# Kernel tuning notes

Measured on AMD Instinct MI355X. Metric: run time of the kernel, lower is better.

The kernel has to match this reference:

```python
import jax, jax.numpy as jnp
import numpy as np

EPS_BN = 1e-5
SLOPE = 0.2
K_SCALES = (5, 20, 30)
K_BRANCH = 20


def _pairwise(x):
    # x: [B, C, N] -> negative squared distances [B, N, N]
    inner = -2.0 * jnp.einsum('bcn,bcm->bnm', x, x)
    xx = jnp.sum(x * x, axis=1)  # [B, N]
    return -xx[:, :, None] - inner - xx[:, None, :]


def _gather(xt, idx):
    # xt: [B, N, C], idx: [B, N, k] -> [B, N, k, C]
    B = xt.shape[0]
    return xt[jnp.arange(B)[:, None, None], idx]


def _bn(x, g, b):
    # eval-mode BN: running_mean=0, running_var=1
    sh = (1, -1) + (1,) * (x.ndim - 2)
    return x * (g / jnp.sqrt(1.0 + EPS_BN)).reshape(sh) + b.reshape(sh)


def _conv(x, w, g, b):
    # 1x1 conv (no bias) + BN + LeakyReLU; x: [B, Cin, ...], w: [Cout, Cin]
    y = jnp.einsum('oc,bc...->bo...', w, x)
    return jax.nn.leaky_relu(_bn(y, g, b), SLOPE)


def _edge_feature(x, k):
    # DGCNN edge feature: cat(neighbor - center, center) -> [B, 2C, N, k]
    idx = jax.lax.top_k(_pairwise(x), k)[1]
    xt = jnp.transpose(x, (0, 2, 1))  # [B, N, C]
    nb = _gather(xt, idx)             # [B, N, k, C]
    ctr = jnp.broadcast_to(xt[:, :, None, :], nb.shape)
    return jnp.transpose(jnp.concatenate([nb - ctr, ctr], axis=-1), (0, 3, 1, 2))


def _hierarchical_features(x):
    pd = _pairwise(x)
    xt = jnp.transpose(x, (0, 2, 1))  # [B, N, 3]
    feats = []
    for scale, k in enumerate(K_SCALES):
        idx = jax.lax.top_k(pd, k)[1]
        nb = _gather(xt, idx)
        ctr = jnp.broadcast_to(xt[:, :, None, :], nb.shape)
        rel = nb - ctr
        if scale == 0:
            f = jnp.concatenate([rel, ctr], axis=-1)                         # 6 ch
        elif scale == 1:
            n = jnp.linalg.norm(rel, axis=-1, keepdims=True) + 1e-8
            f = jnp.concatenate([rel, rel / n, ctr], axis=-1)                # 9 ch
        else:
            d = jnp.linalg.norm(rel, axis=-1, keepdims=True)
            f = jnp.concatenate([rel, ctr, d], axis=-1)                      # 7 ch
        feats.append(jnp.transpose(f, (0, 3, 1, 2)))  # [B, C, N, k]
    return feats


def _forward(x, w1l, g1l, b1l, w1b, g1b, b1b, w1c, g1c, b1c,
             wf, gf, bf, w2, g2, b2, w3, g3, b3, w4, g4, b4,
             w5, g5, b5, wl1, g6, b6, wl2, bl2, g7, b7, wl3, bl3):
    fL, fB, fC = _hierarchical_features(x)
    xl = jnp.max(_conv(fL, w1l, g1l, b1l), axis=-1)   # [B, 64, N]
    xb = jnp.max(_conv(fB, w1b, g1b, b1b), axis=-1)
    xc = jnp.max(_conv(fC, w1c, g1c, b1c), axis=-1)
    xm = jnp.concatenate([xl, xb, xc], axis=1)        # [B, 192, N]
    x1 = _conv(xm, wf, gf, bf)                        # [B, 64, N]
    e = _edge_feature(x1, K_BRANCH)
    x2 = jnp.max(_conv(e, w2, g2, b2), axis=-1)       # [B, 64, N]
    e = _edge_feature(x2, K_BRANCH)
    x3 = jnp.max(_conv(e, w3, g3, b3), axis=-1)       # [B, 128, N]
    e = _edge_feature(x3, K_BRANCH)
    x4 = jnp.max(_conv(e, w4, g4, b4), axis=-1)       # [B, 256, N]
    xcat = jnp.concatenate([x1, x2, x3, x4], axis=1)  # [B, 512, N]
    x5 = _conv(xcat, w5, g5, b5)                      # [B, emb, N]
    h = jnp.concatenate([jnp.max(x5, axis=-1), jnp.mean(x5, axis=-1)], axis=1)  # [B, 2*emb]
    h = jax.nn.leaky_relu(_bn(h @ wl1.T, g6, b6), SLOPE)          # [B, 512]
    h = jax.nn.leaky_relu(_bn(h @ wl2.T + bl2, g7, b7), SLOPE)    # [B, 256]
    return h @ wl3.T + bl3                                        # [B, 7]


def setup_inputs() -> dict:
    key = jax.random.key(0)
    ks = jax.random.split(key, 64)
    it = iter(range(64))
    def W(shape):
        return 0.05 * jax.random.normal(ks[next(it)], shape, jnp.float32)
    def G(n):
        return 1.0 + 0.1 * jax.random.normal(ks[next(it)], (n,), jnp.float32)
    def Bt(n):
        return 0.1 * jax.random.normal(ks[next(it)], (n,), jnp.float32)
    emb = 1024
    inp = {
        'x': jax.random.normal(ks[next(it)], (16, 3, 2048), jnp.float32),
        'w1l': W((64, 6)),  'g1l': G(64),  'b1l': Bt(64),
        'w1b': W((64, 9)),  'g1b': G(64),  'b1b': Bt(64),
        'w1c': W((64, 7)),  'g1c': G(64),  'b1c': Bt(64),
        'wf': W((64, 192)), 'gf': G(64),   'bf': Bt(64),
        'w2': W((64, 128)), 'g2': G(64),   'b2': Bt(64),
        'w3': W((128, 128)),'g3': G(128),  'b3': Bt(128),
        'w4': W((256, 256)),'g4': G(256),  'b4': Bt(256),
        'w5': W((emb, 512)),'g5': G(emb),  'b5': Bt(emb),
        'wl1': W((512, 2 * emb)), 'g6': G(512), 'b6': Bt(512),
        'wl2': W((256, 512)), 'bl2': Bt(256), 'g7': G(256), 'b7': Bt(256),
        'wl3': W((7, 256)), 'bl3': Bt(7),
    }
    return inp


def reference(x, w1l, g1l, b1l, w1b, g1b, b1b, w1c, g1c, b1c,
              wf, gf, bf, w2, g2, b2, w3, g3, b3, w4, g4, b4,
              w5, g5, b5, wl1, g6, b6, wl2, bl2, g7, b7, wl3, bl3):
    return _forward(x, w1l, g1l, b1l, w1b, g1b, b1b, w1c, g1c, b1c,
                    wf, gf, bf, w2, g2, b2, w3, g3, b3, w4, g4, b4,
                    w5, g5, b5, wl1, g6, b6, wl2, bl2, g7, b7, wl3, bl3)
```

## Files before the change

kernel.cpp:

```cpp
#include <hip/hip_runtime.h>
#include <math.h>

#define BB 16
#define NN 2048
#define BN (BB * NN)
#define XS 512

typedef unsigned short u16;
typedef __attribute__((ext_vector_type(8))) short short8;
typedef __attribute__((ext_vector_type(4))) float f32x4;

__device__ __forceinline__ float leaky(float z) { return z > 0.f ? z : 0.2f * z; }
__device__ __forceinline__ float bnscale(float g) { return g / sqrtf(1.f + 1e-5f); }

template<int K>
__device__ __forceinline__ void wave_topk(float lv[32], int lane, int* out) {
    unsigned pop = 0u;
    float v1 = -INFINITY, v2 = -INFINITY, v3 = -INFINITY;
    int m1 = 0, m2 = 0, m3 = 0;
    #pragma unroll
    for (int m = 0; m < 32; ++m) {
        float v = lv[m];
        bool c1 = v > v1, c2 = v > v2, c3 = v > v3;
        v3 = c2 ? v2 : (c3 ? v : v3);
        m3 = c2 ? m2 : (c3 ? m : m3);
        v2 = c1 ? v1 : (c2 ? v : v2);
        m2 = c1 ? m1 : (c2 ? m : m2);
        v1 = c1 ? v : v1;
        m1 = c1 ? m : m1;
    }
    int nvalid = 3;
    #pragma unroll 1
    for (int k = 0; k < K; k += 2) {
        float a1 = v1, a2 = v2;
        int   g1 = m1 * 64 + lane, g2 = m2 * 64 + lane;
        #pragma unroll
        for (int off = 1; off < 64; off <<= 1) {
            float b1 = __shfl_xor(a1, off), b2 = __shfl_xor(a2, off);
            int   h1 = __shfl_xor(g1, off), h2 = __shfl_xor(g2, off);
            bool aw = (a1 > b1) || (a1 == b1 && g1 < h1);
            float w1  = aw ? a1 : b1;  int wi1 = aw ? g1 : h1;
            float lo  = aw ? b1 : a1;  int loi = aw ? h1 : g1;
            float ws  = aw ? a2 : b2;  int wsi = aw ? g2 : h2;
            bool sw = (lo > ws) || (lo == ws && loi < wsi);
            a1 = w1; g1 = wi1;
            a2 = sw ? lo : ws; g2 = sw ? loi : wsi;
        }
        if (lane == 0) {
            out[k] = g1;
            if (k + 1 < K) out[k + 1] = g2;
        }
        if (k + 2 >= K) break;
        const int myg1 = m1 * 64 + lane, myg2 = m2 * 64 + lane;
        const bool p1 = (myg1 == g1) || (myg1 == g2);
        const bool p2 = (myg2 == g1) || (myg2 == g2);
        if (p1) pop |= 1u << m1;
        if (p2) pop |= 1u << m2;
        const int np = (int)p1 + (int)p2;
        if (np == 2) {
            v1 = v3; m1 = m3;
        } else if (p1) {
            v1 = v2; m1 = m2; v2 = v3; m2 = m3;
        } else if (p2) {
            v2 = v3; m2 = m3;
        }
        nvalid -= np;
        if (nvalid < 2) {
            v1 = -INFINITY; v2 = -INFINITY; v3 = -INFINITY;
            m1 = 0; m2 = 0; m3 = 0;
            #pragma unroll
            for (int m = 0; m < 32; ++m) {
                float v = ((pop >> m) & 1u) ? -INFINITY : lv[m];
                bool c1 = v > v1, c2 = v > v2, c3 = v > v3;
                v3 = c2 ? v2 : (c3 ? v : v3);
                m3 = c2 ? m2 : (c3 ? m : m3);
                v2 = c1 ? v1 : (c2 ? v : v2);
                m2 = c1 ? m1 : (c2 ? m : m2);
                v1 = c1 ? v : v1;
                m1 = c1 ? m : m1;
            }
            nvalid = 3;
        }
    }
}

__global__ __launch_bounds__(256) void topk_xyz(const float* __restrict__ x,
                                                int* __restrict__ idx30) {
    const int tile = blockIdx.x;
    const int b = tile >> 9;
    const int i0 = (tile & 511) * 4;
    __shared__ float dist[4][NN];
    const float* xb = x + (size_t)b * 3 * NN;
    float xi[4][3], ni[4];
    #pragma unroll
    for (int t = 0; t < 4; ++t) {
        xi[t][0] = xb[i0 + t];
        xi[t][1] = xb[NN + i0 + t];
        xi[t][2] = xb[2 * NN + i0 + t];
        ni[t] = xi[t][0] * xi[t][0] + xi[t][1] * xi[t][1] + xi[t][2] * xi[t][2];
    }
    for (int j = threadIdx.x; j < NN; j += 256) {
        float a0 = xb[j], a1 = xb[NN + j], a2 = xb[2 * NN + j];
        float nj = a0 * a0 + a1 * a1 + a2 * a2;
        #pragma unroll
        for (int t = 0; t < 4; ++t) {
            float dot = xi[t][0] * a0 + xi[t][1] * a1 + xi[t][2] * a2;
            dist[t][j] = 2.f * dot - ni[t] - nj;
        }
    }
    __syncthreads();
    const int w = threadIdx.x >> 6;
    const int lane = threadIdx.x & 63;
    float lv[32];
    #pragma unroll
    for (int m = 0; m < 32; ++m) lv[m] = dist[w][m * 64 + lane];
    wave_topk<30>(lv, lane, idx30 + ((size_t)b * NN + i0 + w) * 30);
}

__global__ __launch_bounds__(64) void hier_conv(
        const float* __restrict__ x, const int* __restrict__ idx30,
        const float* __restrict__ w1l, const float* __restrict__ g1l, const float* __restrict__ b1l,
        const float* __restrict__ w1b, const float* __restrict__ g1b, const float* __restrict__ b1b,
        const float* __restrict__ w1c, const float* __restrict__ g1c, const float* __restrict__ b1c,
        const float* __restrict__ wf,  const float* __restrict__ gf,  const float* __restrict__ bf_,
        float* __restrict__ x1out) {
    const int bi = blockIdx.x;
    const int b = bi >> 11;
    const int i = bi & (NN - 1);
    const int o = threadIdx.x;
    __shared__ float xm[192];
    __shared__ float xjs[30][3];
    const float* xb = x + (size_t)b * 3 * NN;
    float xi0 = xb[i], xi1 = xb[NN + i], xi2 = xb[2 * NN + i];
    if (o < 30) {
        int j = idx30[(size_t)bi * 30 + o];
        xjs[o][0] = xb[j]; xjs[o][1] = xb[NN + j]; xjs[o][2] = xb[2 * NN + j];
    }
    float wl[6], wb[9], wc[7];
    #pragma unroll
    for (int c = 0; c < 6; ++c) wl[c] = w1l[o * 6 + c];
    #pragma unroll
    for (int c = 0; c < 9; ++c) wb[c] = w1b[o * 9 + c];
    #pragma unroll
    for (int c = 0; c < 7; ++c) wc[c] = w1c[o * 7 + c];
    float sl = bnscale(g1l[o]), bl = b1l[o];
    float sb = bnscale(g1b[o]), bbv = b1b[o];
    float sc = bnscale(g1c[o]), bc = b1c[o];
    __syncthreads();
    float aL = -INFINITY, aB = -INFINITY, aC = -INFINITY;
    for (int k = 0; k < 30; ++k) {
        float r0 = xjs[k][0] - xi0, r1 = xjs[k][1] - xi1, r2 = xjs[k][2] - xi2;
        float ss = r0 * r0 + r1 * r1 + r2 * r2;
        if (k < 5) {
            float y = wl[0]*r0 + wl[1]*r1 + wl[2]*r2 + wl[3]*xi0 + wl[4]*xi1 + wl[5]*xi2;
            aL = fmaxf(aL, leaky(y * sl + bl));
        }
        if (k < 20) {
            float nrm = sqrtf(ss) + 1e-8f;
            float y = wb[0]*r0 + wb[1]*r1 + wb[2]*r2
                    + wb[3]*(r0/nrm) + wb[4]*(r1/nrm) + wb[5]*(r2/nrm)
                    + wb[6]*xi0 + wb[7]*xi1 + wb[8]*xi2;
            aB = fmaxf(aB, leaky(y * sb + bbv));
        }
        {
            float d = sqrtf(ss);
            float y = wc[0]*r0 + wc[1]*r1 + wc[2]*r2 + wc[3]*xi0 + wc[4]*xi1 + wc[5]*xi2 + wc[6]*d;
            aC = fmaxf(aC, leaky(y * sc + bc));
        }
    }
    xm[o] = aL; xm[64 + o] = aB; xm[128 + o] = aC;
    __syncthreads();
    const float* wr = wf + (size_t)o * 192;
    float y = 0.f;
    #pragma unroll 8
    for (int c = 0; c < 192; c += 4) {
        float4 wv = *(const float4*)(wr + c);
        float4 xv = *(const float4*)(&xm[c]);
        y += wv.x * xv.x + wv.y * xv.y + wv.z * xv.z + wv.w * xv.w;
    }
    y = leaky(y * bnscale(gf[o]) + bf_[o]);
    x1out[(size_t)bi * XS + o] = y;
}

template<int C>
__global__ __launch_bounds__(256) void rownorm(const float* __restrict__ xin,
                                               float* __restrict__ nrm) {
    int i = blockIdx.x * 256 + threadIdx.x;
    const float* r = xin + (size_t)i * XS;
    float s = 0.f;
    #pragma unroll 4
    for (int c = 0; c < C; c += 4) {
        float4 v = *(const float4*)(r + c);
        s += v.x * v.x + v.y * v.y + v.z * v.z + v.w * v.w;
    }
    nrm[i] = s;
}

template<int C>
__global__ __launch_bounds__(256) void transpose_feat(const float* __restrict__ xin,
                                                      float* __restrict__ xT) {
    const int blk = blockIdx.x;
    const int b = blk >> 5;
    const int i0 = (blk & 31) * 64;
    const int it = threadIdx.x & 63;
    const int cg = threadIdx.x >> 6;
    const int i = i0 + it;
    const float* row = xin + (size_t)(b * NN + i) * XS;
    float* xTb = xT + (size_t)b * C * NN;
    #pragma unroll 1
    for (int c = cg * (C / 4); c < (cg + 1) * (C / 4); c += 4) {
        float4 v = *(const float4*)(row + c);
        xTb[(size_t)(c + 0) * NN + i] = v.x;
        xTb[(size_t)(c + 1) * NN + i] = v.y;
        xTb[(size_t)(c + 2) * NN + i] = v.z;
        xTb[(size_t)(c + 3) * NN + i] = v.w;
    }
}

template<int C>
__global__ __launch_bounds__(256, 2) void topk_feat(const float* __restrict__ xin,
                                                    const float* __restrict__ nrm,
                                                    int* __restrict__ idx20) {
    const int i0 = blockIdx.x * 8;
    const int b = i0 >> 11;
    const int li0 = i0 & (NN - 1);
    __shared__ float dist[8][NN];
    const int tid = threadIdx.x;
    const float* xb = xin + (size_t)b * NN * XS;
    const float* xi_g = xb + (size_t)li0 * XS;
    float ni[8];
    #pragma unroll
    for (int t = 0; t < 8; ++t) ni[t] = nrm[b * NN + li0 + t];
    #pragma unroll 1
    for (int s = 0; s < 2; ++s) {
        const int j0 = tid + 1024 * s;
        float nj[4];
        #pragma unroll
        for (int q = 0; q < 4; ++q) nj[q] = nrm[b * NN + j0 + 256 * q];
        float acc[8][4];
        #pragma unroll
        for (int t = 0; t < 8; ++t)
            #pragma unroll
            for (int q = 0; q < 4; ++q) acc[t][q] = 0.f;
        #pragma unroll 1
        for (int c = 0; c < C; c += 16) {
            float4 v[4][4];
            #pragma unroll
            for (int q = 0; q < 4; ++q) {
                const float* xj = xb + (size_t)(j0 + 256 * q) * XS + c;
                v[q][0] = *(const float4*)(xj);
                v[q][1] = *(const float4*)(xj + 4);
                v[q][2] = *(const float4*)(xj + 8);
                v[q][3] = *(const float4*)(xj + 12);
            }
            #pragma unroll
            for (int t = 0; t < 8; ++t) {
                const float* xr = xi_g + (size_t)t * XS + c;
                float4 a0 = *(const float4*)(xr);
                float4 a1 = *(const float4*)(xr + 4);
                float4 a2 = *(const float4*)(xr + 8);
                float4 a3 = *(const float4*)(xr + 12);
                #pragma unroll
                for (int q = 0; q < 4; ++q) {
                    float sum = acc[t][q];
                    sum += a0.x * v[q][0].x; sum += a0.y * v[q][0].y;
                    sum += a0.z * v[q][0].z; sum += a0.w * v[q][0].w;
                    sum += a1.x * v[q][1].x; sum += a1.y * v[q][1].y;
                    sum += a1.z * v[q][1].z; sum += a1.w * v[q][1].w;
                    sum += a2.x * v[q][2].x; sum += a2.y * v[q][2].y;
                    sum += a2.z * v[q][2].z; sum += a2.w * v[q][2].w;
                    sum += a3.x * v[q][3].x; sum += a3.y * v[q][3].y;
                    sum += a3.z * v[q][3].z; sum += a3.w * v[q][3].w;
                    acc[t][q] = sum;
                }
            }
        }
        #pragma unroll
        for (int t = 0; t < 8; ++t)
            #pragma unroll
            for (int q = 0; q < 4; ++q)
                dist[t][j0 + 256 * q] = 2.f * acc[t][q] - ni[t] - nj[q];
    }
    __syncthreads();
    const int w = tid >> 6;
    const int lane = tid & 63;
    #pragma unroll 1
    for (int rr = 0; rr < 2; ++rr) {
        const int t = w + 4 * rr;
        float lv[32];
        #pragma unroll
        for (int m = 0; m < 32; ++m) lv[m] = dist[t][m * 64 + lane];
        wave_topk<20>(lv, lane, idx20 + (size_t)(i0 + t) * 20);
    }
}

template<int C>
__global__ __launch_bounds__(512, 4) void topk_feat_t(
        const float* __restrict__ xin, const float* __restrict__ xT,
        const float* __restrict__ nrm, int* __restrict__ idx20) {
    const int i0 = blockIdx.x * 8;
    const int b = i0 >> 11;
    const int li0 = i0 & (NN - 1);
    __shared__ float dist[8][NN];
    __shared__ float xi[8][C];
    const int tid = threadIdx.x;
    for (int t4 = tid * 4; t4 < 8 * C; t4 += 2048) {
        const int t = t4 / C, c = t4 % C;
        *(float4*)&xi[t][c] = *(const float4*)&xin[(size_t)(i0 + t) * XS + c];
    }
    float ni[8];
    #pragma unroll
    for (int t = 0; t < 8; ++t) ni[t] = nrm[b * NN + li0 + t];
    const float4 nj = *(const float4*)&nrm[b * NN + tid * 4];
    const float* xTb = xT + (size_t)b * C * NN;
    __syncthreads();
    float acc[8][4];
    #pragma unroll
    for (int t = 0; t < 8; ++t)
        #pragma unroll
        for (int j = 0; j < 4; ++j) acc[t][j] = 0.f;
    #pragma unroll 1
    for (int c0 = 0; c0 < C; c0 += 4) {
        float4 vj[4];
        #pragma unroll
        for (int cc = 0; cc < 4; ++cc)
            vj[cc] = *(const float4*)&xTb[(size_t)(c0 + cc) * NN + tid * 4];
        #pragma unroll
        for (int t = 0; t < 8; ++t) {
            const float4 av = *(const float4*)&xi[t][c0];
            acc[t][0] += av.x * vj[0].x;
            acc[t][1] += av.x * vj[0].y;
            acc[t][2] += av.x * vj[0].z;
            acc[t][3] += av.x * vj[0].w;
            acc[t][0] += av.y * vj[1].x;
            acc[t][1] += av.y * vj[1].y;
            acc[t][2] += av.y * vj[1].z;
            acc[t][3] += av.y * vj[1].w;
            acc[t][0] += av.z * vj[2].x;
            acc[t][1] += av.z * vj[2].y;
            acc[t][2] += av.z * vj[2].z;
            acc[t][3] += av.z * vj[2].w;
            acc[t][0] += av.w * vj[3].x;
            acc[t][1] += av.w * vj[3].y;
            acc[t][2] += av.w * vj[3].z;
            acc[t][3] += av.w * vj[3].w;
        }
    }
    #pragma unroll
    for (int t = 0; t < 8; ++t) {
        float4 d;
        d.x = 2.f * acc[t][0] - ni[t] - nj.x;
        d.y = 2.f * acc[t][1] - ni[t] - nj.y;
        d.z = 2.f * acc[t][2] - ni[t] - nj.z;
        d.w = 2.f * acc[t][3] - ni[t] - nj.w;
        *(float4*)&dist[t][tid * 4] = d;
    }
    __syncthreads();
    const int w = tid >> 6;
    const int lane = tid & 63;
    float lv[32];
    #pragma unroll
    for (int m = 0; m < 32; ++m) lv[m] = dist[w][m * 64 + lane];
    wave_topk<20>(lv, lane, idx20 + (size_t)(i0 + w) * 20);
}

template<int C, int COUT>
__global__ __launch_bounds__(256) void pconv(
        const float* __restrict__ xin,
        const float* __restrict__ w,
        float* __restrict__ pt) {
    constexpr int O2 = 2 * COUT;
    constexpr int PB = 8192 / O2;
    constexpr int OG = O2 / 8;
    constexpr int PG = PB / 4;
    static_assert(OG * PG == 256, "tile mismatch");
    const int i0 = blockIdx.x * PB;
    __shared__ __align__(16) float xt[PB][C + 4];
    const int tid = threadIdx.x;
    for (int t = tid * 4; t < PB * C; t += 1024)
        *(float4*)(&xt[t / C][t % C]) =
            *(const float4*)(&xin[(size_t)(i0 + t / C) * XS + (t % C)]);
    __syncthreads();
    const int og = tid % OG, pg = tid / OG;
    const int o0 = og * 8, p0 = pg * 4;
    const bool thalf = (o0 >= COUT);
    const float* wb0 = w + (size_t)(thalf ? o0 - COUT : o0) * 2 * C;
    float acc[8][4];
    #pragma unroll
    for (int r = 0; r < 8; ++r)
        #pragma unroll
        for (int p = 0; p < 4; ++p) acc[r][p] = 0.f;
    #pragma unroll 2
    for (int c = 0; c < C; c += 4) {
        float4 wf[8];
        if (thalf) {
            #pragma unroll
            for (int r = 0; r < 8; ++r) {
                float4 a = *(const float4*)(wb0 + (size_t)r * 2 * C + c);
                float4 bq = *(const float4*)(wb0 + (size_t)r * 2 * C + C + c);
                wf[r].x = bq.x - a.x; wf[r].y = bq.y - a.y;
                wf[r].z = bq.z - a.z; wf[r].w = bq.w - a.w;
            }
        } else {
            #pragma unroll
            for (int r = 0; r < 8; ++r)
                wf[r] = *(const float4*)(wb0 + (size_t)r * 2 * C + c);
        }
        #pragma unroll
        for (int p = 0; p < 4; ++p) {
            float4 xv = *(const float4*)(&xt[p0 + p][c]);
            #pragma unroll
            for (int r = 0; r < 8; ++r)
                acc[r][p] += wf[r].x * xv.x + wf[r].y * xv.y
                           + wf[r].z * xv.z + wf[r].w * xv.w;
        }
    }
    #pragma unroll
    for (int p = 0; p < 4; ++p) {
        float* dst = pt + (size_t)(i0 + p0 + p) * O2 + o0;
        *(float4*)(dst)     = make_float4(acc[0][p], acc[1][p], acc[2][p], acc[3][p]);
        *(float4*)(dst + 4) = make_float4(acc[4][p], acc[5][p], acc[6][p], acc[7][p]);
    }
}

template<int COUT>
__global__ __launch_bounds__(256) void gmax(
        const float* __restrict__ pt, const int* __restrict__ idx20,
        const float* __restrict__ g, const float* __restrict__ bb,
        float* __restrict__ xout) {
    constexpr int TPP = COUT / 4;
    constexpr int PTS = 256 / TPP;
    const int i0 = blockIdx.x * PTS;
    const int base = i0 & ~(NN - 1);
    __shared__ int jl[PTS][20];
    const int tid = threadIdx.x;
    for (int t = tid; t < PTS * 20; t += 256)
        jl[t / 20][t % 20] = idx20[(size_t)(i0 + t / 20) * 20 + (t % 20)];
    __syncthreads();
    const int p = tid / TPP;
    const int q = (tid % TPP) * 4;
    const int i = i0 + p;
    float4 mx = make_float4(-INFINITY, -INFINITY, -INFINITY, -INFINITY);
    float4 mn = make_float4(INFINITY, INFINITY, INFINITY, INFINITY);
    #pragma unroll 4
    for (int k = 0; k < 20; ++k) {
        float4 v = *(const float4*)(pt + (size_t)(base + jl[p][k]) * (2 * COUT) + q);
        mx.x = fmaxf(mx.x, v.x); mx.y = fmaxf(mx.y, v.y);
        mx.z = fmaxf(mx.z, v.z); mx.w = fmaxf(mx.w, v.w);
        mn.x = fminf(mn.x, v.x); mn.y = fminf(mn.y, v.y);
        mn.z = fminf(mn.z, v.z); mn.w = fminf(mn.w, v.w);
    }
    float4 tv = *(const float4*)(pt + (size_t)i * (2 * COUT) + COUT + q);
    float4 gv = *(const float4*)(g + q);
    float4 bv = *(const float4*)(bb + q);
    float4 res;
    {
        float s = bnscale(gv.x); res.x = leaky(((s >= 0.f ? mx.x : mn.x) + tv.x) * s + bv.x);
    }{
        float s = bnscale(gv.y); res.y = leaky(((s >= 0.f ? mx.y : mn.y) + tv.y) * s + bv.y);
    }{
        float s = bnscale(gv.z); res.z = leaky(((s >= 0.f ? mx.z : mn.z) + tv.z) * s + bv.z);
    }{
        float s = bnscale(gv.w); res.w = leaky(((s >= 0.f ? mx.w : mn.w) + tv.w) * s + bv.w);
    }
    *(float4*)(xout + (size_t)i * XS + q) = res;
}

__global__ __launch_bounds__(256) void split_bf16(const float* __restrict__ in,
                                                  u16* __restrict__ hi,
                                                  u16* __restrict__ lo, int n4) {
    int i = blockIdx.x * 256 + threadIdx.x;
    if (i >= n4) return;
    float4 v = ((const float4*)in)[i];
    float vv[4] = {v.x, v.y, v.z, v.w};
    unsigned h[4], l[4];
    #pragma unroll
    for (int t = 0; t < 4; ++t) {
        unsigned u = __float_as_uint(vv[t]);
        unsigned r = (u + 0x7FFFu + ((u >> 16) & 1u)) >> 16;
        h[t] = r;
        float res = vv[t] - __uint_as_float(r << 16);
        unsigned u2 = __float_as_uint(res);
        l[t] = (u2 + 0x7FFFu + ((u2 >> 16) & 1u)) >> 16;
    }
    ((uint2*)hi)[i] = make_uint2(h[0] | (h[1] << 16), h[2] | (h[3] << 16));
    ((uint2*)lo)[i] = make_uint2(l[0] | (l[1] << 16), l[2] | (l[3] << 16));
}

__global__ __launch_bounds__(256) void conv5_mfma2(
        const u16* __restrict__ xhi, const u16* __restrict__ xlo,
        const u16* __restrict__ whi, const u16* __restrict__ wlo,
        const float* __restrict__ g5, const float* __restrict__ b5,
        float* __restrict__ pmax, float* __restrict__ psum) {
    const int mblk = blockIdx.x >> 2;
    const int nblk = blockIdx.x & 3;
    const int wv = threadIdx.x >> 6;
    const int lane = threadIdx.x & 63;
    const int row = lane & 15;
    const int quad = lane >> 4;
    const int m0 = mblk * 64;
    const int n0 = nblk * 256 + wv * 64;
    const u16* xh = xhi + (size_t)(m0 + row) * 512 + quad * 8;
    const u16* xl = xlo + (size_t)(m0 + row) * 512 + quad * 8;
    const u16* wh = whi + (size_t)(n0 + row) * 512 + quad * 8;
    const u16* wl = wlo + (size_t)(n0 + row) * 512 + quad * 8;
    f32x4 acc[4][4];
    #pragma unroll
    for (int f = 0; f < 4; ++f)
        #pragma unroll
        for (int g = 0; g < 4; ++g) acc[f][g] = (f32x4){0.f, 0.f, 0.f, 0.f};
    #pragma unroll 1
    for (int k = 0; k < 512; k += 32) {
        short8 ah[4], al[4], bh[4], bl[4];
        #pragma unroll
        for (int f = 0; f < 4; ++f) {
            ah[f] = *(const short8*)(xh + (size_t)f * 16 * 512 + k);
            al[f] = *(const short8*)(xl + (size_t)f * 16 * 512 + k);
        }
        #pragma unroll
        for (int g = 0; g < 4; ++g) {
            bh[g] = *(const short8*)(wh + (size_t)g * 16 * 512 + k);
            bl[g] = *(const short8*)(wl + (size_t)g * 16 * 512 + k);
        }
        #pragma unroll
        for (int f = 0; f < 4; ++f)
            #pragma unroll
            for (int g = 0; g < 4; ++g) {
                acc[f][g] = __builtin_amdgcn_mfma_f32_16x16x32_bf16(ah[f], bh[g], acc[f][g], 0, 0, 0);
                acc[f][g] = __builtin_amdgcn_mfma_f32_16x16x32_bf16(ah[f], bl[g], acc[f][g], 0, 0, 0);
                acc[f][g] = __builtin_amdgcn_mfma_f32_16x16x32_bf16(al[f], bh[g], acc[f][g], 0, 0, 0);
            }
    }
    const int b = m0 >> 11;
    const int ch0 = (m0 & (NN - 1)) >> 4;
    #pragma unroll
    for (int f = 0; f < 4; ++f) {
        const int ch = ch0 + f;
        #pragma unroll
        for (int g = 0; g < 4; ++g) {
            const int oc = n0 + g * 16 + row;
            float s = bnscale(g5[oc]), bv = b5[oc];
            float mx = -INFINITY, sm = 0.f;
            #pragma unroll
            for (int r = 0; r < 4; ++r) {
                float z = leaky(acc[f][g][r] * s + bv);
                mx = fmaxf(mx, z); sm += z;
            }
            mx = fmaxf(mx, __shfl_xor(mx, 16)); sm += __shfl_xor(sm, 16);
            mx = fmaxf(mx, __shfl_xor(mx, 32)); sm += __shfl_xor(sm, 32);
            if (lane < 16) {
                pmax[((size_t)b * 128 + ch) * 1024 + oc] = mx;
                psum[((size_t)b * 128 + ch) * 1024 + oc] = sm;
            }
        }
    }
}

__global__ __launch_bounds__(256, 3) void conv5_pool(
        const float* __restrict__ xcat,
        const float* __restrict__ w5, const float* __restrict__ g5,
        const float* __restrict__ b5,
        float* __restrict__ pmax, float* __restrict__ psum) {
    const int blk = blockIdx.x;
    const int b = blk >> 6;
    const int ch = blk & 63;
    const int i0 = ch * 32;
    const float* xrow = xcat + ((size_t)b * NN + i0) * XS;
    const int tid = threadIdx.x;
    float acc[4][32];
    #pragma unroll
    for (int q = 0; q < 4; ++q)
        #pragma unroll
        for (int p = 0; p < 32; ++p) acc[q][p] = 0.f;
    #pragma unroll 1
    for (int c = 0; c < 512; c += 4) {
        float4 wv[4];
        #pragma unroll
        for (int q = 0; q < 4; ++q)
            wv[q] = *(const float4*)(w5 + (size_t)(tid + 256 * q) * 512 + c);
        #pragma unroll
        for (int p = 0; p < 32; ++p) {
            float4 xs = *(const float4*)(xrow + (size_t)p * XS + c);
            #pragma unroll
            for (int q = 0; q < 4; ++q)
                acc[q][p] += wv[q].x * xs.x + wv[q].y * xs.y
                           + wv[q].z * xs.z + wv[q].w * xs.w;
        }
    }
    #pragma unroll
    for (int q = 0; q < 4; ++q) {
        int oc = tid + 256 * q;
        float s = bnscale(g5[oc]), bv = b5[oc];
        float m = -INFINITY, sm = 0.f;
        #pragma unroll
        for (int p = 0; p < 32; ++p) {
            float z = leaky(acc[q][p] * s + bv);
            m = fmaxf(m, z);
            sm += z;
        }
        pmax[((size_t)b * 64 + ch) * 1024 + oc] = m;
        psum[((size_t)b * 64 + ch) * 1024 + oc] = sm;
    }
}

__global__ __launch_bounds__(256) void pool_reduce(
        const float* __restrict__ pmax, const float* __restrict__ psum,
        int nch, float* __restrict__ hbuf) {
    const int b = blockIdx.x >> 3;
    const int g = blockIdx.x & 7;
    const int tid = threadIdx.x;
    const int oc = g * 128 + (tid & 127);
    const int half = tid >> 7;
    const int h0 = half * (nch / 2);
    float m = -INFINITY, sm = 0.f;
    for (int ch = h0; ch < h0 + nch / 2; ++ch) {
        m = fmaxf(m, pmax[((size_t)b * nch + ch) * 1024 + oc]);
        sm += psum[((size_t)b * nch + ch) * 1024 + oc];
    }
    __shared__ float sx[128], ss[128];
    if (half == 1) { sx[tid & 127] = m; ss[tid & 127] = sm; }
    __syncthreads();
    if (half == 0) {
        m = fmaxf(m, sx[tid & 127]);
        sm += ss[tid & 127];
        hbuf[(size_t)b * 2048 + oc] = m;
        hbuf[(size_t)b * 2048 + 1024 + oc] = sm * (1.0f / 2048.0f);
    }
}

__global__ __launch_bounds__(256) void fc_head(
        const float* __restrict__ hbuf,
        const float* __restrict__ wl1, const float* __restrict__ g6, const float* __restrict__ b6,
        const float* __restrict__ wl2, const float* __restrict__ bl2,
        const float* __restrict__ g7, const float* __restrict__ b7,
        const float* __restrict__ wl3, const float* __restrict__ bl3,
        float* __restrict__ out) {
    const int b = blockIdx.x;
    const int tid = threadIdx.x;
    __shared__ float h[2048];
    __shared__ float h1[512];
    __shared__ float h2[256];
    for (int t = tid * 4; t < 2048; t += 1024)
        *(float4*)(&h[t]) = *(const float4*)(hbuf + (size_t)b * 2048 + t);
    __syncthreads();
    #pragma unroll
    for (int q = 0; q < 2; ++q) {
        int o = tid + 256 * q;
        const float* wr = wl1 + (size_t)o * 2048;
        float y = 0.f;
        for (int c = 0; c < 2048; c += 4) {
            float4 wv = *(const float4*)(wr + c);
            float4 hv = *(const float4*)(&h[c]);
            y += wv.x * hv.x + wv.y * hv.y + wv.z * hv.z + wv.w * hv.w;
        }
        y = y * bnscale(g6[o]) + b6[o];
        h1[o] = leaky(y);
    }
    __syncthreads();
    {
        int o = tid;
        const float* wr = wl2 + (size_t)o * 512;
        float y = 0.f;
        for (int c = 0; c < 512; c += 4) {
            float4 wv = *(const float4*)(wr + c);
            float4 hv = *(const float4*)(&h1[c]);
            y += wv.x * hv.x + wv.y * hv.y + wv.z * hv.z + wv.w * hv.w;
        }
        y = (y + bl2[o]) * bnscale(g7[o]) + b7[o];
        h2[o] = leaky(y);
    }
    __syncthreads();
    if (tid < 7) {
        const float* wr = wl3 + tid * 256;
        float y = 0.f;
        for (int c = 0; c < 256; ++c) y += wr[c] * h2[c];
        out[b * 7 + tid] = y + bl3[tid];
    }
}

extern "C" void kernel_launch(void* const* d_in, const int* in_sizes, int n_in,
                              void* d_out, int out_size, void* d_ws, size_t ws_size,
                              hipStream_t stream) {
    const float* x   = (const float*)d_in[0];
    const float* w1l = (const float*)d_in[1];
    const float* g1l = (const float*)d_in[2];
    const float* b1l = (const float*)d_in[3];
    const float* w1b = (const float*)d_in[4];
    const float* g1b = (const float*)d_in[5];
    const float* b1b = (const float*)d_in[6];
    const float* w1c = (const float*)d_in[7];
    const float* g1c = (const float*)d_in[8];
    const float* b1c = (const float*)d_in[9];
    const float* wf  = (const float*)d_in[10];
    const float* gf  = (const float*)d_in[11];
    const float* bf_ = (const float*)d_in[12];
    const float* w2  = (const float*)d_in[13];
    const float* g2  = (const float*)d_in[14];
    const float* b2  = (const float*)d_in[15];
    const float* w3  = (const float*)d_in[16];
    const float* g3  = (const float*)d_in[17];
    const float* b3  = (const float*)d_in[18];
    const float* w4  = (const float*)d_in[19];
    const float* g4  = (const float*)d_in[20];
    const float* b4  = (const float*)d_in[21];
    const float* w5  = (const float*)d_in[22];
    const float* g5  = (const float*)d_in[23];
    const float* b5  = (const float*)d_in[24];
    const float* wl1 = (const float*)d_in[25];
    const float* g6  = (const float*)d_in[26];
    const float* b6  = (const float*)d_in[27];
    const float* wl2 = (const float*)d_in[28];
    const float* bl2 = (const float*)d_in[29];
    const float* g7  = (const float*)d_in[30];
    const float* b7  = (const float*)d_in[31];
    const float* wl3 = (const float*)d_in[32];
    const float* bl3 = (const float*)d_in[33];
    float* out = (float*)d_out;

    char* ws = (char*)d_ws;
    int*   idxb = (int*)(ws);
    float* xcat = (float*)(ws + ((size_t)4  << 20));
    float* nrm  = (float*)(ws + ((size_t)68 << 20));
    float* hbuf = (float*)(ws + ((size_t)68 << 20) + ((size_t)256 << 10));
    float* pt   = (float*)(ws + ((size_t)69 << 20));
    float* xT   = (float*)(ws + ((size_t)69 << 20));
    const bool mfma_ok = ws_size >= ((size_t)151 << 20);
    u16* xlo = (u16*)(ws + ((size_t)69  << 20));
    u16* xhi = (u16*)(ws + ((size_t)101 << 20));
    u16* whi = (u16*)(ws + ((size_t)133 << 20));
    u16* wlo = (u16*)(ws + ((size_t)134 << 20));
    float* pmax = mfma_ok ? (float*)(ws + ((size_t)135 << 20))
                          : (float*)(ws + ((size_t)69 << 20));
    float* psum = mfma_ok ? (float*)(ws + ((size_t)143 << 20))
                          : (float*)(ws + ((size_t)73 << 20));
    const int nch = mfma_ok ? 128 : 64;
    float* x1 = xcat;
    float* x2 = xcat + 64;
    float* x3 = xcat + 128;
    float* x4 = xcat + 256;

    topk_xyz<<<BB * NN / 4, 256, 0, stream>>>(x, idxb);
    hier_conv<<<BB * NN, 64, 0, stream>>>(x, idxb, w1l, g1l, b1l, w1b, g1b, b1b,
                                          w1c, g1c, b1c, wf, gf, bf_, x1);
    rownorm<64><<<BN / 256, 256, 0, stream>>>(x1, nrm);
    if (mfma_ok) {
        transpose_feat<64><<<BB * 32, 256, 0, stream>>>(x1, xT);
        topk_feat_t<64><<<BN / 8, 512, 0, stream>>>(x1, xT, nrm, idxb);
    } else {
        topk_feat<64><<<BN / 8, 256, 0, stream>>>(x1, nrm, idxb);
    }
    pconv<64, 64><<<BN / 64, 256, 0, stream>>>(x1, w2, pt);
    gmax<64><<<BN / 16, 256, 0, stream>>>(pt, idxb, g2, b2, x2);
    rownorm<64><<<BN / 256, 256, 0, stream>>>(x2, nrm);
    if (mfma_ok) {
        transpose_feat<64><<<BB * 32, 256, 0, stream>>>(x2, xT);
        topk_feat_t<64><<<BN / 8, 512, 0, stream>>>(x2, xT, nrm, idxb);
    } else {
        topk_feat<64><<<BN / 8, 256, 0, stream>>>(x2, nrm, idxb);
    }
    pconv<64, 128><<<BN / 32, 256, 0, stream>>>(x2, w3, pt);
    gmax<128><<<BN / 8, 256, 0, stream>>>(pt, idxb, g3, b3, x3);
    rownorm<128><<<BN / 256, 256, 0, stream>>>(x3, nrm);
    if (mfma_ok) {
        transpose_feat<128><<<BB * 32, 256, 0, stream>>>(x3, xT);
        topk_feat_t<128><<<BN / 8, 512, 0, stream>>>(x3, xT, nrm, idxb);
    } else {
        topk_feat<128><<<BN / 8, 256, 0, stream>>>(x3, nrm, idxb);
    }
    for (int h = 0; h < 2; ++h) {
        pconv<128, 128><<<BN / 32, 256, 0, stream>>>(x3, w4 + (size_t)h * 128 * 256, pt);
        gmax<128><<<BN / 8, 256, 0, stream>>>(pt, idxb, g4 + h * 128, b4 + h * 128,
                                              x4 + h * 128);
    }
    if (mfma_ok) {
        split_bf16<<<(BN * 512 / 4) / 256, 256, 0, stream>>>(xcat, xhi, xlo, BN * 512 / 4);
        split_bf16<<<(1024 * 512 / 4) / 256, 256, 0, stream>>>(w5, whi, wlo, 1024 * 512 / 4);
        conv5_mfma2<<<(BN / 64) * 4, 256, 0, stream>>>(xhi, xlo, whi, wlo,
                                                       g5, b5, pmax, psum);
    } else {
        conv5_pool<<<BB * 64, 256, 0, stream>>>(xcat, w5, g5, b5, pmax, psum);
    }
    pool_reduce<<<BB * 8, 256, 0, stream>>>(pmax, psum, nch, hbuf);
    fc_head<<<BB, 256, 0, stream>>>(hbuf, wl1, g6, b6, wl2, bl2,
                                    g7, b7, wl3, bl3, out);
}
```

Baseline: 2.566 ms.

## Replace per-pair wave butterfly reduction with bitonic-sorted key list and insertion updates

The wave-level top-k selection used to run a full 6-step butterfly reduction for every pair of outputs. It now packs value and index into a 64-bit sortable key and bitonic-sorts the per-lane best candidates across the wave once. Each step afterwards takes lane 0's key, refills only from the lane that owned the winner, and shifts the refill into the sorted list with one shuffle-down and compare. This cuts the shuffle work per selected neighbor, at the cost of 64-bit shuffles and one output per iteration instead of two.

```diff
diff --git a/kernel.cpp b/kernel.cpp
--- a/kernel.cpp
+++ b/kernel.cpp
@@ -13,8 +13,15 @@
 __device__ __forceinline__ float leaky(float z) { return z > 0.f ? z : 0.2f * z; }
 __device__ __forceinline__ float bnscale(float g) { return g / sqrtf(1.f + 1e-5f); }
 
+__device__ __forceinline__ unsigned long long topk_key(float v, int gid) {
+    unsigned b = __float_as_uint(v + 0.0f);
+    unsigned u = b ^ ((unsigned)((int)b >> 31) | 0x80000000u);
+    return ((unsigned long long)u << 32) | (unsigned)(~gid);
+}
+
 template<int K>
 __device__ __forceinline__ void wave_topk(float lv[32], int lane, int* out) {
+    static_assert(K <= 31, "pop budget exceeds per-lane candidates");
     unsigned pop = 0u;
     float v1 = -INFINITY, v2 = -INFINITY, v3 = -INFINITY;
     int m1 = 0, m2 = 0, m3 = 0;
@@ -30,42 +37,30 @@
         m1 = c1 ? m : m1;
     }
     int nvalid = 3;
+    unsigned long long key = topk_key(v1, m1 * 64 + lane);
+    #pragma unroll
+    for (int kk = 2; kk <= 64; kk <<= 1) {
+        #pragma unroll
+        for (int j = kk >> 1; j > 0; j >>= 1) {
+            unsigned long long ok = __shfl_xor(key, j);
+            const bool keepMax = ((lane & kk) == 0) == ((lane & j) == 0);
+            key = ((key > ok) == keepMax) ? key : ok;
+        }
+    }
     #pragma unroll 1
-    for (int k = 0; k < K; k += 2) {
-        float a1 = v1, a2 = v2;
-        int   g1 = m1 * 64 + lane, g2 = m2 * 64 + lane;
-        #pragma unroll
-        for (int off = 1; off < 64; off <<= 1) {
-            float b1 = __shfl_xor(a1, off), b2 = __shfl_xor(a2, off);
-            int   h1 = __shfl_xor(g1, off), h2 = __shfl_xor(g2, off);
-            bool aw = (a1 > b1) || (a1 == b1 && g1 < h1);
-            float w1  = aw ? a1 : b1;  int wi1 = aw ? g1 : h1;
-            float lo  = aw ? b1 : a1;  int loi = aw ? h1 : g1;
-            float ws  = aw ? a2 : b2;  int wsi = aw ? g2 : h2;
-            bool sw = (lo > ws) || (lo == ws && loi < wsi);
-            a1 = w1; g1 = wi1;
-            a2 = sw ? lo : ws; g2 = sw ? loi : wsi;
-        }
-        if (lane == 0) {
-            out[k] = g1;
-            if (k + 1 < K) out[k + 1] = g2;
-        }
-        if (k + 2 >= K) break;
-        const int myg1 = m1 * 64 + lane, myg2 = m2 * 64 + lane;
-        const bool p1 = (myg1 == g1) || (myg1 == g2);
-        const bool p2 = (myg2 == g1) || (myg2 == g2);
-        if (p1) pop |= 1u << m1;
-        if (p2) pop |= 1u << m2;
-        const int np = (int)p1 + (int)p2;
-        if (np == 2) {
-            v1 = v3; m1 = m3;
-        } else if (p1) {
+    for (int k = 0; k < K; ++k) {
+        const unsigned long long w = __shfl(key, 0);
+        const int wg = (int)(~(unsigned)w);
+        if (lane == 0) out[k] = wg;
+        if (k + 1 == K) break;
+        const int s = wg & 63;
+        bool need = false;
+        if (lane == s) {
+            pop |= 1u << m1;
             v1 = v2; m1 = m2; v2 = v3; m2 = m3;
-        } else if (p2) {
-            v2 = v3; m2 = m3;
-        }
-        nvalid -= np;
-        if (nvalid < 2) {
+            need = (--nvalid == 0);
+        }
+        if (need) {
             v1 = -INFINITY; v2 = -INFINITY; v3 = -INFINITY;
             m1 = 0; m2 = 0; m3 = 0;
             #pragma unroll
@@ -81,6 +76,11 @@
             }
             nvalid = 3;
         }
+        const unsigned long long e = __shfl(topk_key(v1, m1 * 64 + lane), s);
+        const unsigned long long nb = __shfl_down(key, 1);
+        const bool c1 = (lane < 63) && (nb > e);
+        const bool c2 = (key > e);
+        key = c1 ? nb : (c2 ? e : key);
     }
 }
 
```

Measured after the change: 2.204 ms. 14.1% less time.
